# Performance work log

Measured on AMD Instinct MI355X. Metric: run time of the kernel, lower is better.

Reference implementation:

```python
import jax, jax.numpy as jnp
import numpy as np

N, H, W, C, CK, ITER = 4, 256, 256, 8, 2, 4
HID = 2 * C
C2 = C * C


def project(x, w1, b1, w2, b2, w3, b3):
    # flax Project: Dense->gelu->Dense->gelu->Dense (gelu approximate=tanh, jax default)
    h = jax.nn.gelu(x @ w1 + b1)
    h = jax.nn.gelu(h @ w2 + b2)
    return h @ w3 + b3


def setup_inputs() -> dict:
    key = jax.random.key(0)
    ks = jax.random.split(key, 40)
    d = {}
    d['u'] = jax.random.normal(ks[0], (N, H, W, C), jnp.float32)
    d['k'] = jax.random.normal(ks[1], (N, H, W, CK), jnp.float32)
    idx = 2
    # gamma MLP (in CK), delta MLP (in CK), greens real/imag MLPs (in 2)
    for nm, fin in zip(['g', 'dl', 'fr', 'fi'], [CK, CK, 2, 2]):
        for li, (fi_, fo) in enumerate([(fin, HID), (HID, HID), (HID, C2)]):
            d[f'{nm}_w{li+1}'] = jax.random.normal(ks[idx], (fi_, fo), jnp.float32) / np.sqrt(fi_).astype(np.float32)
            d[f'{nm}_b{li+1}'] = jnp.zeros((fo,), jnp.float32)
            idx += 1
    d['bias'] = jax.random.normal(ks[idx], (C,), jnp.float32)
    return d


def reference(u, k, g_w1, g_b1, g_w2, g_b2, g_w3, g_b3,
              dl_w1, dl_b1, dl_w2, dl_b2, dl_w3, dl_b3,
              fr_w1, fr_b1, fr_w2, fr_b2, fr_w3, fr_b3,
              fi_w1, fi_b1, fi_w2, fi_b2, fi_w3, fi_b3, bias):
    # per-pixel gamma / delta matrices: (N,H,W,C,C), scaled by 1/C^2 as in original
    gmat = (project(k, g_w1, g_b1, g_w2, g_b2, g_w3, g_b3) / C2).reshape(N, H, W, C, C)
    dmat = (project(k, dl_w1, dl_b1, dl_w2, dl_b2, dl_w3, dl_b3) / C2).reshape(N, H, W, C, C)
    # spectral Green's filter on the rfft grid; meshgrid(kx, ky) -> (W, H//2+1)
    kx = jnp.fft.rfftfreq(H, d=1.0 / H)
    ky = jnp.fft.fftfreq(W, d=1.0 / W)
    Kx, Ky = jnp.meshgrid(kx, ky)
    K = jnp.stack([Kx, Ky], axis=-1).astype(jnp.float32)  # (W, H//2+1, 2)
    filt_r = project(K, fr_w1, fr_b1, fr_w2, fr_b2, fr_w3, fr_b3)
    filt_i = project(K, fi_w1, fi_b1, fi_w2, fi_b2, fi_w3, fi_b3)
    filt = ((filt_r + 1j * filt_i) / C2).reshape(W, H // 2 + 1, C, C)  # H==W
    for _ in range(ITER):
        local = 2.0 * u - jnp.einsum('nhwj,nhwjk->nhwk', u, gmat)
        du = jnp.einsum('nhwj,nhwjk->nhwk', u, dmat)
        uf = jnp.fft.rfftn(du, axes=(1, 2))  # (N,H,W//2+1,C) complex
        gu = jnp.fft.irfftn(jnp.einsum('nhwj,hwjk->nhwk', uf, filt), axes=(1, 2))
        u = local + jnp.einsum('nhwj,nhwjk->nhwk', gu, gmat)
    return jax.nn.gelu(u + bias)
```

## Files before the change

kernel.cpp:

```cpp
#include <hip/hip_runtime.h>
#include <math.h>

#define NB 4
#define HB 256
#define WB 256
#define CB 8
#define NPIX (NB*HB*WB)
#define W2B 129
#define TWO_PI_F 6.283185307179586f

typedef float f32x4 __attribute__((ext_vector_type(4)));

__device__ __forceinline__ float gelu_f(float x){
    float z = 0.7978845608028654f*(x + 0.044715f*x*x*x);
    return x / (1.0f + __expf(-2.0f*z));
}

__device__ __forceinline__ unsigned pack_bf16x2(float a, float b){
    unsigned ua = __float_as_uint(a), ub = __float_as_uint(b);
    ua = (ua + 0x7FFFu + ((ua >> 16) & 1u)) >> 16;
    ub = (ub + 0x7FFFu + ((ub >> 16) & 1u)) >> 16;
    return ua | (ub << 16);
}
__device__ __forceinline__ float2 unpack_bf16x2(unsigned v){
    return make_float2(__uint_as_float(v << 16), __uint_as_float(v & 0xFFFF0000u));
}

__device__ __forceinline__ void ldcp(float* dst, const float* __restrict__ src, int n, int t){
    for (int i = t; i < n; i += 256) dst[i] = src[i];
}

__global__ __launch_bounds__(256) void prep_kernel(
    const float* __restrict__ kin,
    const float* gw1,const float* gb1,const float* gw2,const float* gb2,const float* gw3,const float* gb3,
    const float* dw1,const float* db1,const float* dw2,const float* db2,const float* dw3,const float* db3,
    const float* fw1,const float* fb1,const float* fw2,const float* fb2,const float* fw3,const float* fb3,
    const float* iw1,const float* ib1,const float* iw2,const float* ib2,const float* iw3,const float* ib3,
    unsigned* __restrict__ gmat, unsigned* __restrict__ dmat,
    unsigned* __restrict__ fpack)
{
    __shared__ float sw[2816];
    int t = threadIdx.x;
    int b = blockIdx.x;
    if (b < 1024){
        int gd = (b >= 512);
        const float* w1 = gd ? dw1 : gw1;  const float* b1 = gd ? db1 : gb1;
        const float* w2 = gd ? dw2 : gw2;  const float* b2 = gd ? db2 : gb2;
        const float* w3 = gd ? dw3 : gw3;  const float* b3 = gd ? db3 : gb3;
        ldcp(sw+0,   w1,  32, t); ldcp(sw+32,  b1, 16, t);
        ldcp(sw+48,  w2, 256, t); ldcp(sw+304, b2, 16, t);
        ldcp(sw+320, w3,1024, t); ldcp(sw+1344,b3, 64, t);
        __syncthreads();
        unsigned* mat = gd ? dmat : gmat;
        int bb_ = b & 511;
        float a[2], bv[2]; size_t base[2];
#pragma unroll
        for (int p = 0; p < 2; ++p){
            int pix = bb_*512 + p*256 + t;
            float2 kv = ((const float2*)kin)[pix];
            a[p] = kv.x; bv[p] = kv.y;
            base[p] = (size_t)(pix >> 6)*2048 + (pix & 63);
        }
        float h1[2][16], h2[2][16];
#pragma unroll
        for (int o = 0; o < 16; ++o){
            float wx = sw[o], wy = sw[16+o], bo = sw[32+o];
#pragma unroll
            for (int p = 0; p < 2; ++p) h1[p][o] = gelu_f(a[p]*wx + bv[p]*wy + bo);
        }
#pragma unroll
        for (int o = 0; o < 16; ++o){
            float acc0 = sw[304+o], acc1 = acc0;
#pragma unroll
            for (int i = 0; i < 16; ++i){
                float w = sw[48+i*16+o];
                acc0 += h1[0][i]*w; acc1 += h1[1][i]*w;
            }
            h2[0][o] = gelu_f(acc0); h2[1][o] = gelu_f(acc1);
        }
        const float s = 1.0f/64.0f;
#pragma unroll
        for (int o = 0; o < 64; o += 2){
            float a0[2], a1[2];
#pragma unroll
            for (int p = 0; p < 2; ++p){ a0[p] = sw[1344+o]; a1[p] = sw[1344+o+1]; }
#pragma unroll
            for (int i = 0; i < 16; ++i){
                float w0 = sw[320+i*64+o], w1v = sw[320+i*64+o+1];
#pragma unroll
                for (int p = 0; p < 2; ++p){ a0[p] += h2[p][i]*w0; a1[p] += h2[p][i]*w1v; }
            }
#pragma unroll
            for (int p = 0; p < 2; ++p)
                mat[base[p] + (size_t)(o>>1)*64] = pack_bf16x2(a0[p]*s, a1[p]*s);
        }
    } else {
        ldcp(sw+0,   fw1,  32, t); ldcp(sw+32,  fb1, 16, t);
        ldcp(sw+48,  fw2, 256, t); ldcp(sw+304, fb2, 16, t);
        ldcp(sw+320, fw3,1024, t); ldcp(sw+1344,fb3, 64, t);
        ldcp(sw+1408+0,   iw1,  32, t); ldcp(sw+1408+32,  ib1, 16, t);
        ldcp(sw+1408+48,  iw2, 256, t); ldcp(sw+1408+304, ib2, 16, t);
        ldcp(sw+1408+320, iw3,1024, t); ldcp(sw+1408+1344,ib3, 64, t);
        __syncthreads();
        int w2 = b - 1024;
        float x = (float)w2;
        float y = (float)(t < 128 ? t : t - 256);
        float h1r[16], h1i[16], h2r[16], h2i[16];
#pragma unroll
        for (int o = 0; o < 16; ++o){
            h1r[o] = gelu_f(x*sw[o] + y*sw[16+o] + sw[32+o]);
            h1i[o] = gelu_f(x*sw[1408+o] + y*sw[1408+16+o] + sw[1408+32+o]);
        }
#pragma unroll
        for (int o = 0; o < 16; ++o){
            float ar = sw[304+o], ai = sw[1408+304+o];
#pragma unroll
            for (int i = 0; i < 16; ++i){
                ar += h1r[i]*sw[48+i*16+o];
                ai += h1i[i]*sw[1408+48+i*16+o];
            }
            h2r[o] = gelu_f(ar); h2i[o] = gelu_f(ai);
        }
        unsigned* dst = fpack + (size_t)w2*16384 + t;
        const float s = 1.0f/64.0f;
#pragma unroll
        for (int o = 0; o < 64; ++o){
            float ar = sw[1344+o], ai = sw[1408+1344+o];
#pragma unroll
            for (int i = 0; i < 16; ++i){
                ar += h2r[i]*sw[320+i*64+o];
                ai += h2i[i]*sw[1408+320+i*64+o];
            }
            dst[o*256] = pack_bf16x2(ar*s, ai*s);
        }
    }
}

__device__ __forceinline__ void fft256v(f32x4* xr, f32x4* xi, int t, float sgn)
{
    int n2 = t >> 4, k1 = t & 15;
    float csA, snA; __sincosf(sgn*TWO_PI_F*(float)k1*(1.0f/16.0f), &snA, &csA);
    f32x4 ar = {0.f,0.f,0.f,0.f}, ai = {0.f,0.f,0.f,0.f};
    float cw = 1.f, sw = 0.f;
#pragma unroll
    for (int n1 = 0; n1 < 16; ++n1){
        f32x4 vr = xr[16*n1 + n2], vi = xi[16*n1 + n2];
        ar += vr*cw - vi*sw;
        ai += vr*sw + vi*cw;
        float cn = cw*csA - sw*snA;
        sw = cw*snA + sw*csA; cw = cn;
    }
    float cs2, sn2; __sincosf(sgn*TWO_PI_F*(float)(n2*k1)*(1.0f/256.0f), &sn2, &cs2);
    f32x4 br = ar*cs2 - ai*sn2;
    f32x4 bi = ar*sn2 + ai*cs2;
    __syncthreads();
    xr[t] = br; xi[t] = bi;
    __syncthreads();
    int k1b = t & 15, k2 = t >> 4;
    float csB, snB; __sincosf(sgn*TWO_PI_F*(float)k2*(1.0f/16.0f), &snB, &csB);
    f32x4 yr = {0.f,0.f,0.f,0.f}, yi = {0.f,0.f,0.f,0.f};
    cw = 1.f; sw = 0.f;
#pragma unroll
    for (int n2b = 0; n2b < 16; ++n2b){
        f32x4 br2 = xr[n2b*16 + k1b], bi2 = xi[n2b*16 + k1b];
        yr += br2*cw - bi2*sw;
        yi += br2*sw + bi2*cw;
        float cn = cw*csB - sw*snB;
        sw = cw*snB + sw*csB; cw = cn;
    }
    __syncthreads();
    xr[t] = yr; xi[t] = yi;
    __syncthreads();
}

__device__ __forceinline__ void fwd_store(
    f32x4* XR, f32x4* XI, const float* dv, int t, int n, int h,
    float2* __restrict__ spec)
{
    XR[t] = (f32x4){dv[0],dv[2],dv[4],dv[6]};
    XI[t] = (f32x4){dv[1],dv[3],dv[5],dv[7]};
    __syncthreads();
    fft256v(XR, XI, t, -1.f);
    if (t <= 128){
        int m = (256 - t) & 255;
        f32x4 zr = XR[t], zi = XI[t], yr = XR[m], yi = XI[m];
        float4* dst = (float4*)(spec + (((size_t)n*129 + t)*256 + h)*8);
        dst[0] = make_float4(0.5f*(zr.x+yr.x), 0.5f*(zi.x-yi.x), 0.5f*(zi.x+yi.x), 0.5f*(yr.x-zr.x));
        dst[1] = make_float4(0.5f*(zr.y+yr.y), 0.5f*(zi.y-yi.y), 0.5f*(zi.y+yi.y), 0.5f*(yr.y-zr.y));
        dst[2] = make_float4(0.5f*(zr.z+yr.z), 0.5f*(zi.z-yi.z), 0.5f*(zi.z+yi.z), 0.5f*(yr.z-zr.z));
        dst[3] = make_float4(0.5f*(zr.w+yr.w), 0.5f*(zi.w-yi.w), 0.5f*(zi.w+yi.w), 0.5f*(yr.w-zr.w));
    }
}

__device__ __forceinline__ void inv_fft_to_gu(
    const float2* __restrict__ spec, f32x4* XR, f32x4* XI,
    int t, int n, int h, float* gu)
{
    int w2 = (t <= 128) ? t : 256 - t;
    const float4* rp = (const float4*)(spec + (((size_t)n*129 + w2)*256 + h)*8);
    float4 q0 = rp[0], q1 = rp[1], q2 = rp[2], q3 = rp[3];
    f32x4 xr, xi;
    if (t <= 128){
        xr = (f32x4){q0.x - q0.w, q1.x - q1.w, q2.x - q2.w, q3.x - q3.w};
        xi = (f32x4){q0.y + q0.z, q1.y + q1.z, q2.y + q2.z, q3.y + q3.z};
    } else {
        xr = (f32x4){ q0.x + q0.w,  q1.x + q1.w,  q2.x + q2.w,  q3.x + q3.w};
        xi = (f32x4){-q0.y + q0.z, -q1.y + q1.z, -q2.y + q2.z, -q3.y + q3.z};
    }
    XR[t] = xr; XI[t] = xi;
    __syncthreads();
    fft256v(XR, XI, t, +1.f);
    const float s = 1.0f/65536.0f;
    f32x4 gr = XR[t], gi = XI[t];
    gu[0]=gr.x*s; gu[1]=gi.x*s; gu[2]=gr.y*s; gu[3]=gi.y*s;
    gu[4]=gr.z*s; gu[5]=gi.z*s; gu[6]=gr.w*s; gu[7]=gi.w*s;
}

__global__ __launch_bounds__(256) void fft_fwd_kernel(
    const float* __restrict__ u, const unsigned* __restrict__ dmat,
    float2* __restrict__ spec)
{
    __shared__ f32x4 XR[256], XI[256];
    int t = threadIdx.x, bid = blockIdx.x;
    int n = bid >> 8, h = bid & 255;
    const float* up = u + (size_t)bid*2048 + (size_t)t*8;
    float4 ua = ((const float4*)up)[0], ub = ((const float4*)up)[1];
    float uv[8] = {ua.x,ua.y,ua.z,ua.w, ub.x,ub.y,ub.z,ub.w};
    const unsigned* dp = dmat + ((size_t)bid*4 + (t>>6))*2048 + (t&63);
    float dv[8];
#pragma unroll
    for (int k = 0; k < 8; ++k) dv[k] = 0.f;
#pragma unroll
    for (int j = 0; j < 8; ++j){
        float uj = uv[j];
#pragma unroll
        for (int k2 = 0; k2 < 4; ++k2){
            float2 f = unpack_bf16x2(dp[(j*4+k2)*64]);
            dv[2*k2]   += uj * f.x;
            dv[2*k2+1] += uj * f.y;
        }
    }
    fwd_store(XR, XI, dv, t, n, h, spec);
}

__global__ __launch_bounds__(512) void ffth_mult_kernel(
    float2* __restrict__ spec, const unsigned* __restrict__ fpack)
{
    __shared__ f32x4 XR[2][256], XI[2][256];
    int tid = threadIdx.x;
    int t = tid & 255, g = tid >> 8;
    int c0 = g*4;
    int n = blockIdx.x / 129, w2 = blockIdx.x % 129;
    float2* base = spec + ((size_t)(n*129 + w2))*2048;
    const float4* rp = (const float4*)(base + (size_t)t*8);
    float4 ra = rp[g*2], rb = rp[g*2+1];
    XR[g][t] = (f32x4){ra.x, ra.z, rb.x, rb.z};
    XI[g][t] = (f32x4){ra.y, ra.w, rb.y, rb.w};
    __syncthreads();
    fft256v(XR[g], XI[g], t, -1.f);

    f32x4 s0r = XR[0][t], s1r = XR[1][t], s0i = XI[0][t], s1i = XI[1][t];
    float sr[8] = {s0r.x,s0r.y,s0r.z,s0r.w, s1r.x,s1r.y,s1r.z,s1r.w};
    float si[8] = {s0i.x,s0i.y,s0i.z,s0i.w, s1i.x,s1i.y,s1i.z,s1i.w};
    f32x4 orr = {0.f,0.f,0.f,0.f}, oii = {0.f,0.f,0.f,0.f};
    const unsigned* fp = fpack + (size_t)w2*16384 + t;
#pragma unroll
    for (int j = 0; j < 8; ++j){
        float sjr = sr[j], sji = si[j];
        float2 f0 = unpack_bf16x2(fp[(j*8 + c0 + 0)*256]);
        float2 f1 = unpack_bf16x2(fp[(j*8 + c0 + 1)*256]);
        float2 f2 = unpack_bf16x2(fp[(j*8 + c0 + 2)*256]);
        float2 f3 = unpack_bf16x2(fp[(j*8 + c0 + 3)*256]);
        orr.x += sjr*f0.x - sji*f0.y;  oii.x += sjr*f0.y + sji*f0.x;
        orr.y += sjr*f1.x - sji*f1.y;  oii.y += sjr*f1.y + sji*f1.x;
        orr.z += sjr*f2.x - sji*f2.y;  oii.z += sjr*f2.y + sji*f2.x;
        orr.w += sjr*f3.x - sji*f3.y;  oii.w += sjr*f3.y + sji*f3.x;
    }
    __syncthreads();
    XR[g][t] = orr; XI[g][t] = oii;
    __syncthreads();
    fft256v(XR[g], XI[g], t, +1.f);
    f32x4 vr = XR[g][t], vi = XI[g][t];
    float4* wp = (float4*)(base + (size_t)t*8);
    wp[g*2]   = make_float4(vr.x, vi.x, vr.y, vi.y);
    wp[g*2+1] = make_float4(vr.z, vi.z, vr.w, vi.w);
}

__global__ __launch_bounds__(256) void born_step_kernel(
    float2* __restrict__ spec, const float* __restrict__ u_in,
    float* __restrict__ u_out, const unsigned* __restrict__ gmat,
    const unsigned* __restrict__ dmat)
{
    __shared__ f32x4 XR[256], XI[256];
    int t = threadIdx.x, bid = blockIdx.x;
    int n = bid >> 8, h = bid & 255;
    float gu[8];
    inv_fft_to_gu(spec, XR, XI, t, n, h, gu);

    const float* up = u_in + (size_t)bid*2048 + (size_t)t*8;
    float4 ua = ((const float4*)up)[0], ub = ((const float4*)up)[1];
    float uv[8] = {ua.x,ua.y,ua.z,ua.w, ub.x,ub.y,ub.z,ub.w};
    float e[8], acc[8];
#pragma unroll
    for (int c = 0; c < 8; ++c){ e[c] = gu[c] - uv[c]; acc[c] = 2.0f*uv[c]; }
    const unsigned* gp = gmat + ((size_t)bid*4 + (t>>6))*2048 + (t&63);
#pragma unroll
    for (int j = 0; j < 8; ++j){
        float ej = e[j];
#pragma unroll
        for (int k2 = 0; k2 < 4; ++k2){
            float2 f = unpack_bf16x2(gp[(j*4+k2)*64]);
            acc[2*k2]   += ej * f.x;
            acc[2*k2+1] += ej * f.y;
        }
    }
    float* op = u_out + (size_t)bid*2048 + (size_t)t*8;
    ((float4*)op)[0] = make_float4(acc[0],acc[1],acc[2],acc[3]);
    ((float4*)op)[1] = make_float4(acc[4],acc[5],acc[6],acc[7]);

    const unsigned* dp = dmat + ((size_t)bid*4 + (t>>6))*2048 + (t&63);
    float dv[8];
#pragma unroll
    for (int k = 0; k < 8; ++k) dv[k] = 0.f;
#pragma unroll
    for (int j = 0; j < 8; ++j){
        float uj = acc[j];
#pragma unroll
        for (int k2 = 0; k2 < 4; ++k2){
            float2 f = unpack_bf16x2(dp[(j*4+k2)*64]);
            dv[2*k2]   += uj * f.x;
            dv[2*k2+1] += uj * f.y;
        }
    }
    fwd_store(XR, XI, dv, t, n, h, spec);
}

__global__ __launch_bounds__(256) void final_kernel(
    const float2* __restrict__ spec, const float* __restrict__ u_in,
    const unsigned* __restrict__ gmat, const float* __restrict__ bias,
    float* __restrict__ out)
{
    __shared__ f32x4 XR[256], XI[256];
    int t = threadIdx.x, bid = blockIdx.x;
    int n = bid >> 8, h = bid & 255;
    float gu[8];
    inv_fft_to_gu(spec, XR, XI, t, n, h, gu);

    const float* up = u_in + (size_t)bid*2048 + (size_t)t*8;
    float4 ua = ((const float4*)up)[0], ub = ((const float4*)up)[1];
    float uv[8] = {ua.x,ua.y,ua.z,ua.w, ub.x,ub.y,ub.z,ub.w};
    float e[8], acc[8];
#pragma unroll
    for (int c = 0; c < 8; ++c){ e[c] = gu[c] - uv[c]; acc[c] = 2.0f*uv[c]; }
    const unsigned* gp = gmat + ((size_t)bid*4 + (t>>6))*2048 + (t&63);
#pragma unroll
    for (int j = 0; j < 8; ++j){
        float ej = e[j];
#pragma unroll
        for (int k2 = 0; k2 < 4; ++k2){
            float2 f = unpack_bf16x2(gp[(j*4+k2)*64]);
            acc[2*k2]   += ej * f.x;
            acc[2*k2+1] += ej * f.y;
        }
    }
#pragma unroll
    for (int k = 0; k < 8; ++k) acc[k] = gelu_f(acc[k] + bias[k]);
    float* op = out + (size_t)bid*2048 + (size_t)t*8;
    ((float4*)op)[0] = make_float4(acc[0],acc[1],acc[2],acc[3]);
    ((float4*)op)[1] = make_float4(acc[4],acc[5],acc[6],acc[7]);
}

extern "C" void kernel_launch(void* const* d_in, const int* in_sizes, int n_in,
                              void* d_out, int out_size, void* d_ws, size_t ws_size,
                              hipStream_t stream) {
    const float* u_in = (const float*)d_in[0];
    const float* k_in = (const float*)d_in[1];
    const float* Wp[24];
    for (int i = 0; i < 24; ++i) Wp[i] = (const float*)d_in[2+i];
    const float* bias = (const float*)d_in[26];

    char* base = (char*)d_ws;
    unsigned* gmat  = (unsigned*)(base);
    unsigned* dmat  = (unsigned*)(base + 33554432ull);
    unsigned* fpack = (unsigned*)(base + 67108864ull);
    float*    u_ws  = (float*)   (base + 75563008ull);
    float2*   spec  = (float2*)  (base + 83951616ull);

    prep_kernel<<<1153, 256, 0, stream>>>(k_in,
        Wp[0],Wp[1],Wp[2],Wp[3],Wp[4],Wp[5],
        Wp[6],Wp[7],Wp[8],Wp[9],Wp[10],Wp[11],
        Wp[12],Wp[13],Wp[14],Wp[15],Wp[16],Wp[17],
        Wp[18],Wp[19],Wp[20],Wp[21],Wp[22],Wp[23],
        gmat, dmat, fpack);

    fft_fwd_kernel<<<1024, 256, 0, stream>>>(u_in, dmat, spec);
    for (int it = 0; it < 4; ++it){
        ffth_mult_kernel<<<516, 512, 0, stream>>>(spec, fpack);
        if (it < 3){
            born_step_kernel<<<1024, 256, 0, stream>>>(
                spec, (it == 0) ? u_in : u_ws, u_ws, gmat, dmat);
        } else {
            final_kernel<<<1024, 256, 0, stream>>>(spec, u_ws, gmat, bias, (float*)d_out);
        }
    }
}
```

Baseline: 231.7 us.

## Restructure prep MLP to one pixel per thread with vector LDS loads, trim FFT syncs

The prep kernel now handles one pixel per thread over twice as many blocks, reads weights from shared memory as 4-wide vectors, and schedules the filter blocks first. gelu uses a hardware reciprocal instead of a division. A new FFT core variant returns results in registers, which drops the final shared-memory write-back and barrier in the inverse transforms; one extra barrier is added before the forward store. The aim is lower register pressure and fewer LDS round-trips and syncs, at the cost of more blocks and slightly less exact gelu.

Result: faster. 220.7 us (-4.7%).

```diff
diff --git a/kernel.cpp b/kernel.cpp
--- a/kernel.cpp
+++ b/kernel.cpp
@@ -13,7 +13,7 @@
 
 __device__ __forceinline__ float gelu_f(float x){
     float z = 0.7978845608028654f*(x + 0.044715f*x*x*x);
-    return x / (1.0f + __expf(-2.0f*z));
+    return x * __builtin_amdgcn_rcpf(1.0f + __expf(-2.0f*z));
 }
 
 __device__ __forceinline__ unsigned pack_bf16x2(float a, float b){
@@ -39,11 +39,11 @@
     unsigned* __restrict__ gmat, unsigned* __restrict__ dmat,
     unsigned* __restrict__ fpack)
 {
-    __shared__ float sw[2816];
+    __shared__ __align__(16) float sw[2816];
     int t = threadIdx.x;
     int b = blockIdx.x;
-    if (b < 1024){
-        int gd = (b >= 512);
+    if (b >= 129){
+        int gd = (b >= 1153);
         const float* w1 = gd ? dw1 : gw1;  const float* b1 = gd ? db1 : gb1;
         const float* w2 = gd ? dw2 : gw2;  const float* b2 = gd ? db2 : gb2;
         const float* w3 = gd ? dw3 : gw3;  const float* b3 = gd ? db3 : gb3;
@@ -52,47 +52,35 @@
         ldcp(sw+320, w3,1024, t); ldcp(sw+1344,b3, 64, t);
         __syncthreads();
         unsigned* mat = gd ? dmat : gmat;
-        int bb_ = b & 511;
-        float a[2], bv[2]; size_t base[2];
-#pragma unroll
-        for (int p = 0; p < 2; ++p){
-            int pix = bb_*512 + p*256 + t;
-            float2 kv = ((const float2*)kin)[pix];
-            a[p] = kv.x; bv[p] = kv.y;
-            base[p] = (size_t)(pix >> 6)*2048 + (pix & 63);
-        }
-        float h1[2][16], h2[2][16];
-#pragma unroll
-        for (int o = 0; o < 16; ++o){
-            float wx = sw[o], wy = sw[16+o], bo = sw[32+o];
-#pragma unroll
-            for (int p = 0; p < 2; ++p) h1[p][o] = gelu_f(a[p]*wx + bv[p]*wy + bo);
-        }
-#pragma unroll
-        for (int o = 0; o < 16; ++o){
-            float acc0 = sw[304+o], acc1 = acc0;
+        int pix = (b - (gd ? 1153 : 129))*256 + t;
+        float2 kv = ((const float2*)kin)[pix];
+        size_t base = (size_t)(pix >> 6)*2048 + (pix & 63);
+        float h1[16], h2[16];
+#pragma unroll
+        for (int o = 0; o < 16; ++o)
+            h1[o] = gelu_f(kv.x*sw[o] + kv.y*sw[16+o] + sw[32+o]);
+#pragma unroll
+        for (int oc = 0; oc < 4; ++oc){
+            f32x4 acc = *(const f32x4*)(sw + 304 + oc*4);
 #pragma unroll
             for (int i = 0; i < 16; ++i){
-                float w = sw[48+i*16+o];
-                acc0 += h1[0][i]*w; acc1 += h1[1][i]*w;
+                f32x4 w = *(const f32x4*)(sw + 48 + i*16 + oc*4);
+                acc += h1[i]*w;
             }
-            h2[0][o] = gelu_f(acc0); h2[1][o] = gelu_f(acc1);
+            h2[oc*4+0] = gelu_f(acc.x); h2[oc*4+1] = gelu_f(acc.y);
+            h2[oc*4+2] = gelu_f(acc.z); h2[oc*4+3] = gelu_f(acc.w);
         }
         const float s = 1.0f/64.0f;
 #pragma unroll
-        for (int o = 0; o < 64; o += 2){
-            float a0[2], a1[2];
-#pragma unroll
-            for (int p = 0; p < 2; ++p){ a0[p] = sw[1344+o]; a1[p] = sw[1344+o+1]; }
+        for (int oc = 0; oc < 16; ++oc){
+            f32x4 acc = *(const f32x4*)(sw + 1344 + oc*4);
 #pragma unroll
             for (int i = 0; i < 16; ++i){
-                float w0 = sw[320+i*64+o], w1v = sw[320+i*64+o+1];
-#pragma unroll
-                for (int p = 0; p < 2; ++p){ a0[p] += h2[p][i]*w0; a1[p] += h2[p][i]*w1v; }
+                f32x4 w = *(const f32x4*)(sw + 320 + i*64 + oc*4);
+                acc += h2[i]*w;
             }
-#pragma unroll
-            for (int p = 0; p < 2; ++p)
-                mat[base[p] + (size_t)(o>>1)*64] = pack_bf16x2(a0[p]*s, a1[p]*s);
+            mat[base + (size_t)(oc*2+0)*64] = pack_bf16x2(acc.x*s, acc.y*s);
+            mat[base + (size_t)(oc*2+1)*64] = pack_bf16x2(acc.z*s, acc.w*s);
         }
     } else {
         ldcp(sw+0,   fw1,  32, t); ldcp(sw+32,  fb1, 16, t);
@@ -102,7 +90,7 @@
         ldcp(sw+1408+48,  iw2, 256, t); ldcp(sw+1408+304, ib2, 16, t);
         ldcp(sw+1408+320, iw3,1024, t); ldcp(sw+1408+1344,ib3, 64, t);
         __syncthreads();
-        int w2 = b - 1024;
+        int w2 = b;
         float x = (float)w2;
         float y = (float)(t < 128 ? t : t - 256);
         float h1r[16], h1i[16], h2r[16], h2i[16];
@@ -171,6 +159,42 @@
     __syncthreads();
     xr[t] = yr; xi[t] = yi;
     __syncthreads();
+}
+
+__device__ __forceinline__ void fft256v_core(f32x4* xr, f32x4* xi, int t, float sgn,
+                                             f32x4& outR, f32x4& outI)
+{
+    int n2 = t >> 4, k1 = t & 15;
+    float csA, snA; __sincosf(sgn*TWO_PI_F*(float)k1*(1.0f/16.0f), &snA, &csA);
+    f32x4 ar = {0.f,0.f,0.f,0.f}, ai = {0.f,0.f,0.f,0.f};
+    float cw = 1.f, sw = 0.f;
+#pragma unroll
+    for (int n1 = 0; n1 < 16; ++n1){
+        f32x4 vr = xr[16*n1 + n2], vi = xi[16*n1 + n2];
+        ar += vr*cw - vi*sw;
+        ai += vr*sw + vi*cw;
+        float cn = cw*csA - sw*snA;
+        sw = cw*snA + sw*csA; cw = cn;
+    }
+    float cs2, sn2; __sincosf(sgn*TWO_PI_F*(float)(n2*k1)*(1.0f/256.0f), &sn2, &cs2);
+    f32x4 br = ar*cs2 - ai*sn2;
+    f32x4 bi = ar*sn2 + ai*cs2;
+    __syncthreads();
+    xr[t] = br; xi[t] = bi;
+    __syncthreads();
+    int k1b = t & 15, k2 = t >> 4;
+    float csB, snB; __sincosf(sgn*TWO_PI_F*(float)k2*(1.0f/16.0f), &snB, &csB);
+    f32x4 yr = {0.f,0.f,0.f,0.f}, yi = {0.f,0.f,0.f,0.f};
+    cw = 1.f; sw = 0.f;
+#pragma unroll
+    for (int n2b = 0; n2b < 16; ++n2b){
+        f32x4 br2 = xr[n2b*16 + k1b], bi2 = xi[n2b*16 + k1b];
+        yr += br2*cw - bi2*sw;
+        yi += br2*sw + bi2*cw;
+        float cn = cw*csB - sw*snB;
+        sw = cw*snB + sw*csB; cw = cn;
+    }
+    outR = yr; outI = yi;
 }
 
 __device__ __forceinline__ void fwd_store(
@@ -209,9 +233,9 @@
     }
     XR[t] = xr; XI[t] = xi;
     __syncthreads();
-    fft256v(XR, XI, t, +1.f);
+    f32x4 gr, gi;
+    fft256v_core(XR, XI, t, +1.f, gr, gi);
     const float s = 1.0f/65536.0f;
-    f32x4 gr = XR[t], gi = XI[t];
     gu[0]=gr.x*s; gu[1]=gi.x*s; gu[2]=gr.y*s; gu[3]=gi.y*s;
     gu[4]=gr.z*s; gu[5]=gi.z*s; gu[6]=gr.w*s; gu[7]=gi.w*s;
 }
@@ -257,11 +281,16 @@
     XR[g][t] = (f32x4){ra.x, ra.z, rb.x, rb.z};
     XI[g][t] = (f32x4){ra.y, ra.w, rb.y, rb.w};
     __syncthreads();
-    fft256v(XR[g], XI[g], t, -1.f);
-
-    f32x4 s0r = XR[0][t], s1r = XR[1][t], s0i = XI[0][t], s1i = XI[1][t];
-    float sr[8] = {s0r.x,s0r.y,s0r.z,s0r.w, s1r.x,s1r.y,s1r.z,s1r.w};
-    float si[8] = {s0i.x,s0i.y,s0i.z,s0i.w, s1i.x,s1i.y,s1i.z,s1i.w};
+    f32x4 sR, sI;
+    fft256v_core(XR[g], XI[g], t, -1.f, sR, sI);
+    __syncthreads();
+    XR[g][t] = sR; XI[g][t] = sI;
+    __syncthreads();
+    f32x4 oR = XR[1-g][t], oI = XI[1-g][t];
+    f32x4 aR = g ? oR : sR, aI = g ? oI : sI;
+    f32x4 bR = g ? sR : oR, bI = g ? sI : oI;
+    float sr[8] = {aR.x,aR.y,aR.z,aR.w, bR.x,bR.y,bR.z,bR.w};
+    float si[8] = {aI.x,aI.y,aI.z,aI.w, bI.x,bI.y,bI.z,bI.w};
     f32x4 orr = {0.f,0.f,0.f,0.f}, oii = {0.f,0.f,0.f,0.f};
     const unsigned* fp = fpack + (size_t)w2*16384 + t;
 #pragma unroll
@@ -279,11 +308,11 @@
     __syncthreads();
     XR[g][t] = orr; XI[g][t] = oii;
     __syncthreads();
-    fft256v(XR[g], XI[g], t, +1.f);
-    f32x4 vr = XR[g][t], vi = XI[g][t];
+    f32x4 vR, vI;
+    fft256v_core(XR[g], XI[g], t, +1.f, vR, vI);
     float4* wp = (float4*)(base + (size_t)t*8);
-    wp[g*2]   = make_float4(vr.x, vi.x, vr.y, vi.y);
-    wp[g*2+1] = make_float4(vr.z, vi.z, vr.w, vi.w);
+    wp[g*2]   = make_float4(vR.x, vI.x, vR.y, vI.y);
+    wp[g*2+1] = make_float4(vR.z, vI.z, vR.w, vI.w);
 }
 
 __global__ __launch_bounds__(256) void born_step_kernel(
@@ -332,6 +361,7 @@
             dv[2*k2+1] += uj * f.y;
         }
     }
+    __syncthreads();
     fwd_store(XR, XI, dv, t, n, h, spec);
 }
 
@@ -386,7 +416,7 @@
     float*    u_ws  = (float*)   (base + 75563008ull);
     float2*   spec  = (float2*)  (base + 83951616ull);
 
-    prep_kernel<<<1153, 256, 0, stream>>>(k_in,
+    prep_kernel<<<2177, 256, 0, stream>>>(k_in,
         Wp[0],Wp[1],Wp[2],Wp[3],Wp[4],Wp[5],
         Wp[6],Wp[7],Wp[8],Wp[9],Wp[10],Wp[11],
         Wp[12],Wp[13],Wp[14],Wp[15],Wp[16],Wp[17],
```
